# Optimization experiments

Hardware: AMD Instinct MI355X
Metric: run time of the kernel (lower is better)

Reference implementation:

```python
import jax, jax.numpy as jnp
import numpy as np

B, C, L, H = 4, 512, 2048, 8
DH = C // H
SCALE = DH ** -0.5
EPS = 1e-5  # torch LayerNorm default


def setup_inputs() -> dict:
    key = jax.random.key(0)
    ks = jax.random.split(key, 3)
    x = jax.random.normal(ks[0], (B, C, L), dtype=jnp.float32)
    # Conv1d kernel_size=1 == per-position linear; weights ~ N(0, 1/C)
    w_qkv = jax.random.normal(ks[1], (3 * C, C), dtype=jnp.float32) / np.sqrt(C)
    b_qkv = jnp.zeros((3 * C,), dtype=jnp.float32)
    # NOTE: original uses zero_module(proj_out); random weights used here so the
    # baseline is non-trivial for kernel correctness testing.
    w_proj = jax.random.normal(ks[2], (C, C), dtype=jnp.float32) / np.sqrt(C)
    b_proj = jnp.zeros((C,), dtype=jnp.float32)
    ln_gamma = jnp.ones((C,), dtype=jnp.float32)
    ln_beta = jnp.zeros((C,), dtype=jnp.float32)
    return {"x": x, "ln_gamma": ln_gamma, "ln_beta": ln_beta,
            "w_qkv": w_qkv, "b_qkv": b_qkv, "w_proj": w_proj, "b_proj": b_proj}


def reference(x, ln_gamma, ln_beta, w_qkv, b_qkv, w_proj, b_proj):
    # ChannelNorm: LayerNorm over channel dim. Work in [B, L, C] layout.
    h = jnp.swapaxes(x, 1, 2)                      # [B, L, C]
    mu = jnp.mean(h, axis=-1, keepdims=True)
    var = jnp.mean((h - mu) ** 2, axis=-1, keepdims=True)
    hn = (h - mu) * jax.lax.rsqrt(var + EPS) * ln_gamma + ln_beta

    # QKV 1x1 conv as GEMM: [B, L, 3C]
    qkv = jnp.einsum('blc,dc->bld', hn, w_qkv) + b_qkv
    qkv = qkv.reshape(B, L, 3, H, DH)
    q, k, v = (qkv[:, :, i].transpose(0, 2, 1, 3) for i in range(3))  # [B, H, L, DH]

    # Scaled dot-product attention (full O(L^2) scores, as in source)
    w = jnp.einsum('bhqd,bhkd->bhqk', q, k) * SCALE
    w = jax.nn.softmax(w, axis=-1)
    o = jnp.einsum('bhqk,bhkd->bhqd', w, v)        # [B, H, L, DH]
    o = o.transpose(0, 2, 1, 3).reshape(B, L, C)

    # proj_out 1x1 conv + residual (dropout in eval mode = identity)
    out = jnp.einsum('blc,dc->bld', o, w_proj) + b_proj
    return jnp.swapaxes(out, 1, 2) + x             # [B, C, L]
```

## Files before the change

### kernel.cpp

```cpp
#include <hip/hip_runtime.h>
#include <hip/hip_bf16.h>

typedef __bf16 bf16;
typedef bf16 bf16x8 __attribute__((ext_vector_type(8)));
typedef bf16 bf16x4 __attribute__((ext_vector_type(4)));
typedef float f32x4 __attribute__((ext_vector_type(4)));

constexpr int B = 4, C = 512, L = 2048, H = 8, DH = 64;
constexpr int BL = B * L;
constexpr int BH = B * H;
constexpr int N_QKV = 3 * C;
constexpr float QSCALE = 0.125f * 1.44269504088896f;
constexpr float EPS = 1e-5f;

constexpr size_t SZ = (size_t)BL * C;
constexpr size_t OFF_HN    = 0;
constexpr size_t OFF_WQKV  = OFF_HN    + SZ * 2;
constexpr size_t OFF_WPROJ = OFF_WQKV  + (size_t)N_QKV * C * 2;
constexpr size_t OFF_Q     = OFF_WPROJ + (size_t)C * C * 2;
constexpr size_t OFF_K     = OFF_Q     + SZ * 2;
constexpr size_t OFF_V     = OFF_K     + SZ * 2;
constexpr size_t OFF_O     = OFF_V     + SZ * 2;
constexpr size_t OFF_STATS = OFF_O     + SZ * 2;
constexpr size_t OFF_OPART = OFF_STATS + (size_t)BL * 2 * 4;
constexpr size_t OFF_ML    = OFF_OPART + (size_t)2 * BH * L * DH * 2;

__device__ __forceinline__ bf16x8 ld8(const bf16* p) {
  return *(const bf16x8*)p;
}

__device__ __forceinline__ void gll16(const bf16* g, bf16* l) {
  __builtin_amdgcn_global_load_lds(
      (const __attribute__((address_space(1))) unsigned int*)(const void*)g,
      (__attribute__((address_space(3))) unsigned int*)(void*)l, 16, 0, 0);
}

__device__ __forceinline__ unsigned pack_bf16(float a, float b) {
  unsigned ua = __builtin_bit_cast(unsigned, a) + 0x8000u;
  unsigned ub = __builtin_bit_cast(unsigned, b) + 0x8000u;
  return __builtin_amdgcn_perm(ub, ua, 0x07060302u);
}
__device__ __forceinline__ float bf_lo(unsigned u) { return __builtin_bit_cast(float, u << 16); }
__device__ __forceinline__ float bf_hi(unsigned u) { return __builtin_bit_cast(float, u & 0xFFFF0000u); }

__global__ __launch_bounds__(256) void k_convert_w(const float* __restrict__ wqkv,
                                                   const float* __restrict__ wproj,
                                                   bf16* __restrict__ wqkv_b,
                                                   bf16* __restrict__ wproj_b) {
  int i = blockIdx.x * 256 + threadIdx.x;
  if (i < N_QKV * C) wqkv_b[i] = (bf16)wqkv[i];
  if (i < C * C)     wproj_b[i] = (bf16)wproj[i];
}

__global__ __launch_bounds__(1024) void k_ln(const float* __restrict__ x,
                                             const float* __restrict__ gamma,
                                             const float* __restrict__ beta,
                                             bf16* __restrict__ hn) {
  int blk = blockIdx.x;
  int b = blk >> 6;
  int l0 = (blk & 63) << 5;
  int t = threadIdx.x;
  int ll = t & 31;
  int cg = t >> 5;
  __shared__ float tile[512][33];
  __shared__ float sh_s[32][33];
  __shared__ float sh_q[32][33];
  __shared__ float mu_s[32], rs_s[32];
  const float* xp = x + ((size_t)b * C) * L + l0;
  float s = 0.f, ss = 0.f;
#pragma unroll
  for (int r = 0; r < 16; ++r) {
    int c = cg * 16 + r;
    float v = xp[(size_t)c * L + ll];
    tile[c][ll] = v;
    s += v; ss += v * v;
  }
  sh_s[cg][ll] = s; sh_q[cg][ll] = ss;
  __syncthreads();
  if (t < 32) {
    float ts = 0.f, tq = 0.f;
#pragma unroll
    for (int i = 0; i < 32; ++i) { ts += sh_s[i][t]; tq += sh_q[i][t]; }
    float mu = ts * (1.0f / C);
    float var = tq * (1.0f / C) - mu * mu;
    mu_s[t] = mu;
    rs_s[t] = rsqrtf(var + EPS);
  }
  __syncthreads();
  int c2 = (t & 255) * 2;
  int lgrp = t >> 8;
  float g0 = gamma[c2], g1 = gamma[c2 + 1];
  float b0 = beta[c2],  b1 = beta[c2 + 1];
#pragma unroll
  for (int it = 0; it < 8; ++it) {
    int l = lgrp * 8 + it;
    float mu = mu_s[l], rstd = rs_s[l];
    float v0 = (tile[c2][l]     - mu) * rstd * g0 + b0;
    float v1 = (tile[c2 + 1][l] - mu) * rstd * g1 + b1;
    *(unsigned*)&hn[(size_t)(b * L + l0 + l) * C + c2] = pack_bf16(v0, v1);
  }
}

__global__ __launch_bounds__(256) void k_gemm_qkv(const bf16* __restrict__ hn,
                                                  const bf16* __restrict__ wq,
                                                  const float* __restrict__ bq,
                                                  bf16* __restrict__ qg,
                                                  bf16* __restrict__ kg,
                                                  bf16* __restrict__ vg) {
  int mt = blockIdx.x, nt = blockIdx.y;
  int m0 = mt << 7, n0 = nt << 7;
  int t = threadIdx.x, lane = t & 63, w = t >> 6;
  int mw = w >> 1, nw = w & 1;
  int q4 = lane >> 4, c16 = lane & 15;
  __shared__ __align__(16) char smem[36864];
  bf16* As = (bf16*)smem;
  bf16* Bs = (bf16*)(smem + 16384);

  int goff[4], ldsoff[4];
#pragma unroll
  for (int p = 0; p < 4; ++p) {
    int idx = (p * 4 + w) * 64 + lane;
    int row = idx >> 3, s0 = idx & 7;
    goff[p] = row * C + (s0 ^ (row & 7)) * 8;
    ldsoff[p] = (p * 4 + w) * 512;
  }

  f32x4 acc[4][4];
#pragma unroll
  for (int mi = 0; mi < 4; ++mi)
#pragma unroll
    for (int ni = 0; ni < 4; ++ni) acc[mi][ni] = (f32x4){0.f, 0.f, 0.f, 0.f};

  const bf16* ap = hn + (size_t)m0 * C;
  const bf16* bp = wq + (size_t)n0 * C;
  for (int k0 = 0; k0 < C; k0 += 64) {
    __syncthreads();
#pragma unroll
    for (int p = 0; p < 4; ++p) {
      gll16(ap + k0 + goff[p], As + ldsoff[p]);
      gll16(bp + k0 + goff[p], Bs + ldsoff[p]);
    }
    __syncthreads();
#pragma unroll
    for (int kk2 = 0; kk2 < 2; ++kk2) {
      bf16x8 af[4], bfr[4];
#pragma unroll
      for (int mi = 0; mi < 4; ++mi) {
        int row = mw * 64 + mi * 16 + c16;
        af[mi] = ld8(As + row * 64 + ((kk2 * 4 + q4) ^ (row & 7)) * 8);
      }
#pragma unroll
      for (int ni = 0; ni < 4; ++ni) {
        int row = nw * 64 + ni * 16 + c16;
        bfr[ni] = ld8(Bs + row * 64 + ((kk2 * 4 + q4) ^ (row & 7)) * 8);
      }
#pragma unroll
      for (int mi = 0; mi < 4; ++mi)
#pragma unroll
        for (int ni = 0; ni < 4; ++ni)
          acc[mi][ni] = __builtin_amdgcn_mfma_f32_16x16x32_bf16(af[mi], bfr[ni], acc[mi][ni], 0, 0, 0);
    }
  }
  __syncthreads();

  int i = nt >> 2;
  int h = ((nt & 3) << 1) + nw;
  int b = m0 >> 11;
  int l0 = (m0 & (L - 1)) + mw * 64;
  float bias[4];
#pragma unroll
  for (int ni = 0; ni < 4; ++ni) bias[ni] = bq[n0 + nw * 64 + ni * 16 + c16];
  bf16* Os = (bf16*)(smem + w * 9216);

  if (i == 2) {
#pragma unroll
    for (int mi = 0; mi < 4; ++mi)
#pragma unroll
      for (int ni = 0; ni < 4; ++ni) {
        bf16x4 pk;
#pragma unroll
        for (int r = 0; r < 4; ++r) pk[r] = (bf16)(acc[mi][ni][r] + bias[ni]);
        *(bf16x4*)&Os[(ni * 16 + c16) * 72 + mi * 16 + q4 * 4] = pk;
      }
    __syncthreads();
    const bf16* src = Os + lane * 72;
    bf16* dst = vg + ((size_t)((b * H + h) * DH + lane)) * L + l0;
#pragma unroll
    for (int s = 0; s < 8; ++s)
      *(uint4*)(dst + s * 8) = *(const uint4*)(src + s * 8);
  } else {
    float sc = (i == 0) ? QSCALE : 1.0f;
#pragma unroll
    for (int mi = 0; mi < 4; ++mi)
#pragma unroll
      for (int ni = 0; ni < 4; ++ni)
#pragma unroll
        for (int r = 0; r < 4; ++r)
          Os[(mi * 16 + q4 * 4 + r) * 72 + ni * 16 + c16] = (bf16)((acc[mi][ni][r] + bias[ni]) * sc);
    __syncthreads();
    bf16* dst0 = (i == 0) ? qg : kg;
    const bf16* src = Os + lane * 72;
    bf16* dst = dst0 + ((size_t)((b * H + h) * L + l0 + lane)) * DH;
#pragma unroll
    for (int s = 0; s < 8; ++s)
      *(uint4*)(dst + s * 8) = *(const uint4*)(src + s * 8);
  }
}

__global__ __launch_bounds__(256, 4) void k_attn(const bf16* __restrict__ qg,
                                                 const bf16* __restrict__ kg,
                                                 const bf16* __restrict__ vt,
                                                 bf16* __restrict__ opart,
                                                 float* __restrict__ lsum) {
  int blk = blockIdx.x;
  int js = blk & 1; blk >>= 1;
  int qt = blk & 15; int bh = blk >> 4;
  int t = threadIdx.x, lane = t & 63, w = t >> 6;
  int q4 = lane >> 4, c16 = lane & 15;
  __shared__ __align__(16) bf16 Ks[64][64];
  __shared__ __align__(16) bf16 Vts[64][64];
  __shared__ __align__(16) bf16 Ps[4][16][72];
  const bf16* qptr  = qg + ((size_t)bh * L + qt * 128 + w * 32) * DH;
  const bf16* kptr  = kg + (size_t)bh * L * DH;
  const bf16* vtptr = vt + (size_t)bh * DH * L;

  int ksoff[2], vsoff[2];
#pragma unroll
  for (int p = 0; p < 2; ++p) {
    int ci = p * 256 + w * 64 + lane;
    int row = ci >> 3, s0 = ci & 7;
    int ch = s0 ^ (row & 7);
    ksoff[p] = row * DH + ch * 8;
    vsoff[p] = row * L + ch * 8;
  }
  int sw = c16 & 7;

  bf16x8 qf[2][2];
#pragma unroll
  for (int qb = 0; qb < 2; ++qb)
#pragma unroll
    for (int kk2 = 0; kk2 < 2; ++kk2)
      qf[qb][kk2] = ld8(&qptr[(size_t)(qb * 16 + c16) * DH + kk2 * 32 + q4 * 8]);

  f32x4 o_acc[2][4];
  float l_i[2] = {0.f, 0.f};
#pragma unroll
  for (int qb = 0; qb < 2; ++qb)
#pragma unroll
    for (int db = 0; db < 4; ++db) o_acc[qb][db] = (f32x4){0.f, 0.f, 0.f, 0.f};

  for (int j0 = js * 1024; j0 < js * 1024 + 1024; j0 += 64) {
    __syncthreads();
#pragma unroll
    for (int p = 0; p < 2; ++p) {
      gll16(kptr + (size_t)j0 * DH + ksoff[p], &Ks[0][0]  + (p * 4 + w) * 512);
      gll16(vtptr + j0 + vsoff[p],             &Vts[0][0] + (p * 4 + w) * 512);
    }
    __syncthreads();

    f32x4 s[2][4];
#pragma unroll
    for (int qb = 0; qb < 2; ++qb)
#pragma unroll
      for (int jb = 0; jb < 4; ++jb) s[qb][jb] = (f32x4){0.f, 0.f, 0.f, 0.f};
#pragma unroll
    for (int kk2 = 0; kk2 < 2; ++kk2) {
      int choff = ((kk2 * 4 + q4) ^ sw) * 8;
#pragma unroll
      for (int jb = 0; jb < 4; ++jb) {
        bf16x8 kf = ld8(&Ks[0][0] + (jb * 16 + c16) * 64 + choff);
        s[0][jb] = __builtin_amdgcn_mfma_f32_16x16x32_bf16(kf, qf[0][kk2], s[0][jb], 0, 0, 0);
        s[1][jb] = __builtin_amdgcn_mfma_f32_16x16x32_bf16(kf, qf[1][kk2], s[1][jb], 0, 0, 0);
      }
    }

#pragma unroll
    for (int qb = 0; qb < 2; ++qb) {
      float rs = 0.f;
#pragma unroll
      for (int jb = 0; jb < 4; ++jb)
#pragma unroll
        for (int r = 0; r < 4; ++r) {
          float p_ = __builtin_amdgcn_exp2f(s[qb][jb][r]);
          s[qb][jb][r] = p_;
          rs += p_;
        }
      l_i[qb] += rs;
    }

    bf16x8 vf[2][4];
#pragma unroll
    for (int kk2 = 0; kk2 < 2; ++kk2) {
      int choff = ((kk2 * 4 + q4) ^ sw) * 8;
#pragma unroll
      for (int db = 0; db < 4; ++db)
        vf[kk2][db] = ld8(&Vts[0][0] + (db * 16 + c16) * 64 + choff);
    }

#pragma unroll
    for (int qb = 0; qb < 2; ++qb) {
#pragma unroll
      for (int jb = 0; jb < 4; ++jb) {
        uint2 pk;
        pk.x = pack_bf16(s[qb][jb][0], s[qb][jb][1]);
        pk.y = pack_bf16(s[qb][jb][2], s[qb][jb][3]);
        *(uint2*)&Ps[w][c16][jb * 16 + q4 * 4] = pk;
      }
#pragma unroll
      for (int kk2 = 0; kk2 < 2; ++kk2) {
        bf16x8 pf = ld8(&Ps[w][c16][kk2 * 32 + q4 * 8]);
#pragma unroll
        for (int db = 0; db < 4; ++db)
          o_acc[qb][db] = __builtin_amdgcn_mfma_f32_16x16x32_bf16(vf[kk2][db], pf, o_acc[qb][db], 0, 0, 0);
      }
    }
  }

#pragma unroll
  for (int qb = 0; qb < 2; ++qb) {
    float lf = l_i[qb];
    lf += __shfl_xor(lf, 16, 64);
    lf += __shfl_xor(lf, 32, 64);
    int q = qt * 128 + w * 32 + qb * 16 + c16;
    bf16* op = opart + (((size_t)js * BH + bh) * L + q) * DH;
#pragma unroll
    for (int db = 0; db < 4; ++db) {
      uint2 pk;
      pk.x = pack_bf16(o_acc[qb][db][0], o_acc[qb][db][1]);
      pk.y = pack_bf16(o_acc[qb][db][2], o_acc[qb][db][3]);
      *(uint2*)&op[db * 16 + q4 * 4] = pk;
    }
    if (q4 == 0) lsum[((size_t)js * BH + bh) * L + q] = lf;
  }
}

__global__ __launch_bounds__(256) void k_gemm_proj(const bf16* __restrict__ opart,
                                                   const float* __restrict__ lsum,
                                                   const bf16* __restrict__ wp,
                                                   const float* __restrict__ bp,
                                                   const float* __restrict__ x,
                                                   float* __restrict__ out) {
  int mt = blockIdx.x, nt = blockIdx.y;
  int m0 = mt << 6, n0 = nt << 6;
  int t = threadIdx.x;
  int lane = t & 63, w = t >> 6;
  int q4 = lane >> 4, c16 = lane & 15;
  __shared__ __align__(16) bf16 As[64][72];
  __shared__ __align__(16) bf16 Bs[64][72];
  __shared__ float Ot[64][65];
  __shared__ float invs[64][9];
  int b = m0 >> 11, q0 = m0 & (L - 1);
  for (int i = t; i < 512; i += 256) {
    int row = i >> 3, h = i & 7;
    int bhh = b * 8 + h;
    float l0v = lsum[(size_t)bhh * L + q0 + row];
    float l1v = lsum[((size_t)BH + bhh) * L + q0 + row];
    invs[row][h] = 1.0f / (l0v + l1v);
  }
  f32x4 acc[4];
#pragma unroll
  for (int nb = 0; nb < 4; ++nb) acc[nb] = (f32x4){0.f, 0.f, 0.f, 0.f};

  for (int k0 = 0; k0 < C; k0 += 64) {
    __syncthreads();
    int h = k0 >> 6;
    const bf16* ap0 = opart + ((size_t)(b * 8 + h) * L + q0) * 64;
    const bf16* ap1 = opart + ((size_t)(BH + b * 8 + h) * L + q0) * 64;
#pragma unroll
    for (int p = 0; p < 2; ++p) {
      int idx = p * 256 + t;
      int row = idx >> 3, ch = idx & 7;
      uint4 u0 = *(const uint4*)(ap0 + (size_t)row * 64 + ch * 8);
      uint4 u1 = *(const uint4*)(ap1 + (size_t)row * 64 + ch * 8);
      float inv = invs[row][h];
      unsigned* pu0 = (unsigned*)&u0;
      unsigned* pu1 = (unsigned*)&u1;
      uint4 m;
      unsigned* pm = (unsigned*)&m;
#pragma unroll
      for (int k = 0; k < 4; ++k)
        pm[k] = pack_bf16((bf_lo(pu0[k]) + bf_lo(pu1[k])) * inv,
                          (bf_hi(pu0[k]) + bf_hi(pu1[k])) * inv);
      *(uint4*)&As[row][ch * 8] = m;
      *(bf16x8*)&Bs[row][ch * 8] = ld8(&wp[(size_t)(n0 + row) * C + k0 + ch * 8]);
    }
    __syncthreads();
#pragma unroll
    for (int kk = 0; kk < 64; kk += 32) {
      bf16x8 a = ld8(&As[w * 16 + c16][kk + q4 * 8]);
#pragma unroll
      for (int nb = 0; nb < 4; ++nb) {
        bf16x8 bfr = ld8(&Bs[nb * 16 + c16][kk + q4 * 8]);
        acc[nb] = __builtin_amdgcn_mfma_f32_16x16x32_bf16(a, bfr, acc[nb], 0, 0, 0);
      }
    }
  }
  __syncthreads();
#pragma unroll
  for (int nb = 0; nb < 4; ++nb)
#pragma unroll
    for (int r = 0; r < 4; ++r)
      Ot[w * 16 + q4 * 4 + r][nb * 16 + c16] = acc[nb][r];
  __syncthreads();
#pragma unroll
  for (int r = 0; r < 16; ++r) {
    int cl = w * 16 + r;
    int c = n0 + cl;
    size_t idx = (size_t)(b * C + c) * L + q0 + lane;
    out[idx] = Ot[lane][cl] + bp[c] + x[idx];
  }
}

extern "C" void kernel_launch(void* const* d_in, const int* in_sizes, int n_in,
                              void* d_out, int out_size, void* d_ws, size_t ws_size,
                              hipStream_t stream) {
  const float* x     = (const float*)d_in[0];
  const float* gamma = (const float*)d_in[1];
  const float* beta  = (const float*)d_in[2];
  const float* wqkv  = (const float*)d_in[3];
  const float* bqkv  = (const float*)d_in[4];
  const float* wproj = (const float*)d_in[5];
  const float* bproj = (const float*)d_in[6];
  float* out = (float*)d_out;
  char* ws = (char*)d_ws;
  bf16* hn  = (bf16*)(ws + OFF_HN);
  bf16* wqb = (bf16*)(ws + OFF_WQKV);
  bf16* wpb = (bf16*)(ws + OFF_WPROJ);
  bf16* qbp = (bf16*)(ws + OFF_Q);
  bf16* kbp = (bf16*)(ws + OFF_K);
  bf16* vbp = (bf16*)(ws + OFF_V);
  bf16* opart = (bf16*)(ws + OFF_OPART);
  float* lsum = (float*)(ws + OFF_ML);

  hipLaunchKernelGGL(k_convert_w, dim3((N_QKV * C + 255) / 256), dim3(256), 0, stream,
                     wqkv, wproj, wqb, wpb);
  hipLaunchKernelGGL(k_ln, dim3(B * (L / 32)), dim3(1024), 0, stream,
                     x, gamma, beta, hn);
  hipLaunchKernelGGL(k_gemm_qkv, dim3(BL / 128, N_QKV / 128), dim3(256), 0, stream,
                     hn, wqb, bqkv, qbp, kbp, vbp);
  hipLaunchKernelGGL(k_attn, dim3(B * H * (L / 128) * 2), dim3(256), 0, stream,
                     qbp, kbp, vbp, opart, lsum);
  hipLaunchKernelGGL(k_gemm_proj, dim3(BL / 64, C / 64), dim3(256), 0, stream,
                     opart, lsum, wpb, bproj, x, out);
}
```

Measured before the change: 174.3 us.

## Split attention key tile across waves and keep P in registers

The attention kernel now gives each block 64 queries instead of 128, and each wave handles a 16-key slice of every 64-key tile for all 64 queries, rather than its own 32 queries against all keys. The softmax probabilities feed directly into a 16x16x16 MFMA as register operands, which removes the LDS round-trip through the Ps buffer. Because each wave holds partial output sums, a three-phase LDS reduction combines them across waves at the end, and row sums are reduced through LDS as well. This doubles the grid and cuts per-iteration LDS traffic, at the cost of a reduction epilogue, more accumulator registers and a smaller MFMA shape for PV.

Result: slower. 226.5 us (+29.9%).

```diff
diff --git a/kernel.cpp b/kernel.cpp
--- a/kernel.cpp
+++ b/kernel.cpp
@@ -5,6 +5,7 @@
 typedef bf16 bf16x8 __attribute__((ext_vector_type(8)));
 typedef bf16 bf16x4 __attribute__((ext_vector_type(4)));
 typedef float f32x4 __attribute__((ext_vector_type(4)));
+typedef short s16x4 __attribute__((ext_vector_type(4)));
 
 constexpr int B = 4, C = 512, L = 2048, H = 8, DH = 64;
 constexpr int BL = B * L;
@@ -214,38 +215,40 @@
                                                  float* __restrict__ lsum) {
   int blk = blockIdx.x;
   int js = blk & 1; blk >>= 1;
-  int qt = blk & 15; int bh = blk >> 4;
+  int qt = blk & 31; int bh = blk >> 5;
   int t = threadIdx.x, lane = t & 63, w = t >> 6;
   int q4 = lane >> 4, c16 = lane & 15;
-  __shared__ __align__(16) bf16 Ks[64][64];
-  __shared__ __align__(16) bf16 Vts[64][64];
-  __shared__ __align__(16) bf16 Ps[4][16][72];
-  const bf16* qptr  = qg + ((size_t)bh * L + qt * 128 + w * 32) * DH;
+  __shared__ __align__(16) char smem[17408];
+  bf16* Ks  = (bf16*)smem;
+  bf16* Vts = (bf16*)(smem + 8192);
+  float* red  = (float*)smem;
+  float* lred = (float*)(smem + 16384);
+  const bf16* qptr  = qg + ((size_t)bh * L + qt * 64) * DH;
   const bf16* kptr  = kg + (size_t)bh * L * DH;
   const bf16* vtptr = vt + (size_t)bh * DH * L;
 
   int ksoff[2], vsoff[2];
 #pragma unroll
   for (int p = 0; p < 2; ++p) {
-    int ci = p * 256 + w * 64 + lane;
-    int row = ci >> 3, s0 = ci & 7;
+    int idx = p * 256 + t;
+    int row = idx >> 3, s0 = idx & 7;
     int ch = s0 ^ (row & 7);
     ksoff[p] = row * DH + ch * 8;
     vsoff[p] = row * L + ch * 8;
   }
   int sw = c16 & 7;
 
-  bf16x8 qf[2][2];
-#pragma unroll
-  for (int qb = 0; qb < 2; ++qb)
+  bf16x8 qf[4][2];
+#pragma unroll
+  for (int qb = 0; qb < 4; ++qb)
 #pragma unroll
     for (int kk2 = 0; kk2 < 2; ++kk2)
       qf[qb][kk2] = ld8(&qptr[(size_t)(qb * 16 + c16) * DH + kk2 * 32 + q4 * 8]);
 
-  f32x4 o_acc[2][4];
-  float l_i[2] = {0.f, 0.f};
-#pragma unroll
-  for (int qb = 0; qb < 2; ++qb)
+  f32x4 o_acc[4][4];
+  float l_i[4] = {0.f, 0.f, 0.f, 0.f};
+#pragma unroll
+  for (int qb = 0; qb < 4; ++qb)
 #pragma unroll
     for (int db = 0; db < 4; ++db) o_acc[qb][db] = (f32x4){0.f, 0.f, 0.f, 0.f};
 
@@ -253,84 +256,86 @@
     __syncthreads();
 #pragma unroll
     for (int p = 0; p < 2; ++p) {
-      gll16(kptr + (size_t)j0 * DH + ksoff[p], &Ks[0][0]  + (p * 4 + w) * 512);
-      gll16(vtptr + j0 + vsoff[p],             &Vts[0][0] + (p * 4 + w) * 512);
-    }
-    __syncthreads();
-
-    f32x4 s[2][4];
-#pragma unroll
-    for (int qb = 0; qb < 2; ++qb)
-#pragma unroll
-      for (int jb = 0; jb < 4; ++jb) s[qb][jb] = (f32x4){0.f, 0.f, 0.f, 0.f};
-#pragma unroll
-    for (int kk2 = 0; kk2 < 2; ++kk2) {
-      int choff = ((kk2 * 4 + q4) ^ sw) * 8;
-#pragma unroll
-      for (int jb = 0; jb < 4; ++jb) {
-        bf16x8 kf = ld8(&Ks[0][0] + (jb * 16 + c16) * 64 + choff);
-        s[0][jb] = __builtin_amdgcn_mfma_f32_16x16x32_bf16(kf, qf[0][kk2], s[0][jb], 0, 0, 0);
-        s[1][jb] = __builtin_amdgcn_mfma_f32_16x16x32_bf16(kf, qf[1][kk2], s[1][jb], 0, 0, 0);
-      }
-    }
-
-#pragma unroll
-    for (int qb = 0; qb < 2; ++qb) {
+      gll16(kptr + (size_t)j0 * DH + ksoff[p], Ks  + (p * 4 + w) * 512);
+      gll16(vtptr + j0 + vsoff[p],             Vts + (p * 4 + w) * 512);
+    }
+    __syncthreads();
+
+    bf16x8 kf[2];
+#pragma unroll
+    for (int kk2 = 0; kk2 < 2; ++kk2)
+      kf[kk2] = ld8(Ks + (w * 16 + c16) * 64 + ((kk2 * 4 + q4) ^ sw) * 8);
+    s16x4 vfrag[4];
+#pragma unroll
+    for (int db = 0; db < 4; ++db) {
+      int row = db * 16 + c16;
+      int ch = ((w * 2 + (q4 >> 1)) ^ (row & 7)) * 8 + (q4 & 1) * 4;
+      vfrag[db] = __builtin_bit_cast(s16x4, *(const bf16x4*)(Vts + row * 64 + ch));
+    }
+
+#pragma unroll
+    for (int qb = 0; qb < 4; ++qb) {
+      f32x4 s = (f32x4){0.f, 0.f, 0.f, 0.f};
+      s = __builtin_amdgcn_mfma_f32_16x16x32_bf16(kf[0], qf[qb][0], s, 0, 0, 0);
+      s = __builtin_amdgcn_mfma_f32_16x16x32_bf16(kf[1], qf[qb][1], s, 0, 0, 0);
       float rs = 0.f;
 #pragma unroll
-      for (int jb = 0; jb < 4; ++jb)
-#pragma unroll
-        for (int r = 0; r < 4; ++r) {
-          float p_ = __builtin_amdgcn_exp2f(s[qb][jb][r]);
-          s[qb][jb][r] = p_;
-          rs += p_;
-        }
+      for (int r = 0; r < 4; ++r) {
+        float p_ = __builtin_amdgcn_exp2f(s[r]);
+        s[r] = p_;
+        rs += p_;
+      }
       l_i[qb] += rs;
-    }
-
-    bf16x8 vf[2][4];
-#pragma unroll
-    for (int kk2 = 0; kk2 < 2; ++kk2) {
-      int choff = ((kk2 * 4 + q4) ^ sw) * 8;
+      uint2 pk;
+      pk.x = pack_bf16(s[0], s[1]);
+      pk.y = pack_bf16(s[2], s[3]);
+      s16x4 pb = __builtin_bit_cast(s16x4, pk);
 #pragma unroll
       for (int db = 0; db < 4; ++db)
-        vf[kk2][db] = ld8(&Vts[0][0] + (db * 16 + c16) * 64 + choff);
-    }
-
-#pragma unroll
-    for (int qb = 0; qb < 2; ++qb) {
-#pragma unroll
-      for (int jb = 0; jb < 4; ++jb) {
-        uint2 pk;
-        pk.x = pack_bf16(s[qb][jb][0], s[qb][jb][1]);
-        pk.y = pack_bf16(s[qb][jb][2], s[qb][jb][3]);
-        *(uint2*)&Ps[w][c16][jb * 16 + q4 * 4] = pk;
-      }
-#pragma unroll
-      for (int kk2 = 0; kk2 < 2; ++kk2) {
-        bf16x8 pf = ld8(&Ps[w][c16][kk2 * 32 + q4 * 8]);
-#pragma unroll
-        for (int db = 0; db < 4; ++db)
-          o_acc[qb][db] = __builtin_amdgcn_mfma_f32_16x16x32_bf16(vf[kk2][db], pf, o_acc[qb][db], 0, 0, 0);
-      }
-    }
-  }
-
-#pragma unroll
-  for (int qb = 0; qb < 2; ++qb) {
+        o_acc[qb][db] = __builtin_amdgcn_mfma_f32_16x16x16bf16_1k(vfrag[db], pb, o_acc[qb][db], 0, 0, 0);
+    }
+  }
+
+#pragma unroll
+  for (int qb = 0; qb < 4; ++qb) {
     float lf = l_i[qb];
     lf += __shfl_xor(lf, 16, 64);
     lf += __shfl_xor(lf, 32, 64);
-    int q = qt * 128 + w * 32 + qb * 16 + c16;
-    bf16* op = opart + (((size_t)js * BH + bh) * L + q) * DH;
-#pragma unroll
-    for (int db = 0; db < 4; ++db) {
-      uint2 pk;
-      pk.x = pack_bf16(o_acc[qb][db][0], o_acc[qb][db][1]);
-      pk.y = pack_bf16(o_acc[qb][db][2], o_acc[qb][db][3]);
-      *(uint2*)&op[db * 16 + q4 * 4] = pk;
-    }
-    if (q4 == 0) lsum[((size_t)js * BH + bh) * L + q] = lf;
+    if (q4 == 0) lred[w * 64 + qb * 16 + c16] = lf;
+  }
+
+#pragma unroll
+  for (int ph = 1; ph < 4; ++ph) {
+    __syncthreads();
+#pragma unroll
+    for (int db = 0; db < 4; ++db)
+      if (((db - w) & 3) == ph)
+#pragma unroll
+        for (int qb = 0; qb < 4; ++qb)
+          *(f32x4*)&red[(db * 4 + qb) * 256 + lane * 4] = o_acc[qb][db];
+    __syncthreads();
+#pragma unroll
+    for (int db = 0; db < 4; ++db)
+      if (db == w)
+#pragma unroll
+        for (int qb = 0; qb < 4; ++qb)
+          o_acc[qb][db] += *(const f32x4*)&red[(db * 4 + qb) * 256 + lane * 4];
+  }
+
+#pragma unroll
+  for (int db = 0; db < 4; ++db)
+    if (db == w)
+#pragma unroll
+      for (int qb = 0; qb < 4; ++qb) {
+        int q = qt * 64 + qb * 16 + c16;
+        uint2 pk;
+        pk.x = pack_bf16(o_acc[qb][db][0], o_acc[qb][db][1]);
+        pk.y = pack_bf16(o_acc[qb][db][2], o_acc[qb][db][3]);
+        *(uint2*)&opart[(((size_t)js * BH + bh) * L + q) * DH + db * 16 + q4 * 4] = pk;
+      }
+  if (w == 0) {
+    float ls = lred[lane] + lred[64 + lane] + lred[128 + lane] + lred[192 + lane];
+    lsum[((size_t)js * BH + bh) * L + qt * 64 + lane] = ls;
   }
 }
 
@@ -438,7 +443,7 @@
                      x, gamma, beta, hn);
   hipLaunchKernelGGL(k_gemm_qkv, dim3(BL / 128, N_QKV / 128), dim3(256), 0, stream,
                      hn, wqb, bqkv, qbp, kbp, vbp);
-  hipLaunchKernelGGL(k_attn, dim3(B * H * (L / 128) * 2), dim3(256), 0, stream,
+  hipLaunchKernelGGL(k_attn, dim3(B * H * (L / 64) * 2), dim3(256), 0, stream,
                      qbp, kbp, vbp, opart, lsum);
   hipLaunchKernelGGL(k_gemm_proj, dim3(BL / 64, C / 64), dim3(256), 0, stream,
                      opart, lsum, wpb, bproj, x, out);
```
